# Optimization experiments

Measured on AMD Instinct MI355X. Metric: run time of the kernel, lower is better.

## Reference

```python
import jax, jax.numpy as jnp
import numpy as np
from jax import lax

B, T, I, H = 64, 512, 256, 512


def _lstm_cell(inp, h, c, Wx, bx, Wh):
    # Wx: (4, in_dim, H), bx: (4, H), Wh: (4, H, H); gate order: i, f, o, g
    gates = jnp.einsum('bi,gio->bgo', inp, Wx) + jnp.einsum('bh,gho->bgo', h, Wh) + bx
    i_t = jax.nn.sigmoid(gates[:, 0])
    f_t = jax.nn.sigmoid(gates[:, 1])
    o_t = jax.nn.sigmoid(gates[:, 2])
    g_t = jnp.tanh(gates[:, 3])
    c_new = f_t * c + i_t * g_t
    h_new = o_t * jnp.tanh(c_new)
    return h_new, c_new


def setup_inputs() -> dict:
    key = jax.random.key(0)
    ks = jax.random.split(key, 9)
    s_i = 1.0 / np.sqrt(H)  # nn.Linear default init scale (uniform fan_in)
    s_x0 = 1.0 / np.sqrt(I)
    u = lambda k, shape, s: jax.random.uniform(k, shape, jnp.float32, -s, s)
    return {
        'x':   jax.random.normal(ks[0], (B, T, I), jnp.float32),
        'Wx0': u(ks[1], (4, I, H), s_x0),
        'bx0': u(ks[2], (4, H), s_x0),
        'Wh0': u(ks[3], (4, H, H), s_i),
        'Wx1': u(ks[4], (4, H, H), s_i),
        'bx1': u(ks[5], (4, H), s_i),
        'Wh1': u(ks[6], (4, H, H), s_i),
        'Wfc': u(ks[7], (H, 1), s_i),
        'bfc': u(ks[8], (1,), s_i),
    }


def reference(x, Wx0, bx0, Wh0, Wx1, bx1, Wh1, Wfc, bfc):
    b = x.shape[0]
    h = Wh0.shape[-1]
    zeros = jnp.zeros((b, h), x.dtype)
    carry0 = (zeros, zeros, zeros, zeros)  # h0, c0, h1, c1

    def step(carry, x_t):
        h0, c0, h1, c1 = carry
        h0, c0 = _lstm_cell(x_t, h0, c0, Wx0, bx0, Wh0)
        h1, c1 = _lstm_cell(h0, h1, c1, Wx1, bx1, Wh1)
        return (h0, c0, h1, c1), None

    x_t_major = jnp.swapaxes(x, 0, 1)  # (T, B, I)
    (h0, c0, h1, c1), _ = lax.scan(step, carry0, x_t_major)
    return h1 @ Wfc + bfc  # (B, 1)
```

## Files before the change

kernel.cpp:

```cpp
#include <hip/hip_runtime.h>
#include <stdint.h>

#define B_ 64
#define T_ 512
#define I_ 256
#define H_ 512
#define NTHR_ 512
#define D_ 8

typedef __attribute__((ext_vector_type(8))) short short8;
typedef __attribute__((ext_vector_type(4))) float float4v;
typedef __attribute__((ext_vector_type(4))) unsigned int uint4v;

static_assert(sizeof(short8) == 16, "");

#define TILE_B 2048
#define SLOT_B ((size_t)4 * 16 * TILE_B)

__device__ __forceinline__ unsigned short f2bf(float x) {
  union { float f; uint32_t u; } v; v.f = x;
  uint32_t r = v.u + 0x7FFFu + ((v.u >> 16) & 1u);
  return (unsigned short)(r >> 16);
}
__device__ __forceinline__ float bf2f(unsigned short h) {
  union { uint32_t u; float f; } v; v.u = ((uint32_t)h) << 16; return v.f;
}
__device__ __forceinline__ void splitHL(float x, unsigned short& hi, unsigned short& lo) {
  hi = f2bf(x);
  lo = f2bf(x - bf2f(hi));
}

__device__ __forceinline__ size_t rbyte(int slot, int bg, int ht) {
  return ((size_t)slot * 64 + bg * 16 + ht) * TILE_B;
}

__device__ __forceinline__ void wait_ge(const uint32_t* p, int tgt) {
  if (tgt <= 0) return;
  int it = 0;
  while ((int)__hip_atomic_load(p, __ATOMIC_RELAXED, __HIP_MEMORY_SCOPE_AGENT) < tgt) {
    if (++it > 2000000) break;
    if (it > 32) __builtin_amdgcn_s_sleep(1);
  }
}

__device__ __forceinline__ short8 mk8(uint32_t a0, uint32_t a1, uint32_t b0, uint32_t b1) {
  union { uint32_t u[4]; short8 s; } t;
  t.u[0] = a0; t.u[1] = a1; t.u[2] = b0; t.u[3] = b1;
  return t.s;
}

#define MFMA16(A, Bv, C) __builtin_amdgcn_mfma_f32_16x16x32_bf16(A, Bv, C, 0, 0, 0)

#define WAITV(n) do { \
    asm volatile("s_waitcnt vmcnt(" #n ")" ::: "memory"); \
    __builtin_amdgcn_sched_barrier(0); \
  } while (0)

template <int LAYER, bool FULL, bool XPK>
__device__ void run_layer(
    int a,
    const float* __restrict__ x,
    const uint8_t* __restrict__ xpk,
    const float* __restrict__ Wxp, const float* __restrict__ bxp,
    const float* __restrict__ Whp,
    uint32_t* prog0, uint32_t* prog1,
    uint8_t* r0, uint8_t* r1,
    float* h1f,
    unsigned short* Wsh, float* red)
{
  constexpr int K1 = LAYER ? H_ : I_;
  constexpr int NT = (K1 + H_) / 32;
  constexpr int NTT = NT / 2;
  const int tid = threadIdx.x;
  const int lane = tid & 63;
  const int wid = tid >> 6;
  const int bg = wid & 3;
  const int kh = wid >> 2;
  const int qq = lane >> 4;
  const int cc = lane & 15;
  const int brow = bg * 16 + cc;

  short8 wlo[NTT];
  for (int pass = 0; pass < 2; ++pass) {
    for (int idx = tid; idx < NT * 512; idx += NTHR_) {
      int tile = idx >> 9, r = idx & 511, ln = r >> 3, j = r & 7;
      int k = tile * 32 + 4 * (ln >> 4) + (j & 3) + 16 * (j >> 2);
      int n = 4 * a + (ln & 3);
      int g = (ln & 15) >> 2;
      float wvv = (k < K1) ? Wxp[((size_t)g * K1 + k) * H_ + n]
                           : Whp[((size_t)g * H_ + (k - K1)) * H_ + n];
      unsigned short hi, lo; splitHL(wvv, hi, lo);
      Wsh[idx] = pass ? hi : lo;
    }
    __syncthreads();
    if (pass == 0) {
      #pragma unroll
      for (int tt = 0; tt < NTT; ++tt) {
        int tile = 2 * tt + kh;
        wlo[tt] = *(const short8*)(Wsh + tile * 512 + lane * 8);
      }
      __syncthreads();
    }
  }

  const float biasv = bxp[(size_t)(cc >> 2) * H_ + 4 * a + (cc & 3)];
  float cst[4] = {0.f, 0.f, 0.f, 0.f};

  uint32_t* myprog = LAYER ? prog1 : prog0;
  const bool ownw = FULL ? ((tid & 127) == a) : false;

  for (int t = 0; t < T_; ++t) {
    const int slotP = FULL ? t       : (t & (D_ - 1));
    const int slotC = FULL ? (t + 1) : ((t + 1) & (D_ - 1));
    const float bv = (kh == 0) ? biasv : 0.f;
    float4v accA = {bv, bv, bv, bv};
    float4v accB = {0.f, 0.f, 0.f, 0.f};
    float4v accC = {0.f, 0.f, 0.f, 0.f};

    uint4v X0[8], X1[8];

    auto issue_ring = [&](int tt) {
      const int tile = 2 * tt + kh;
      const uint8_t* p;
      if (!LAYER)         p = r0 + rbyte(slotP, bg, tile - 8);
      else if (tile < 16) p = r0 + rbyte(slotC, bg, tile);
      else                p = r1 + rbyte(slotP, bg, tile - 16);
      p += (size_t)lane * 16;
      const int s = tt & 7;
      if constexpr (FULL) {
        asm volatile("global_load_dwordx4 %0, %2, off\n\t"
                     "global_load_dwordx4 %1, %2, off offset:1024"
                     : "=&v"(X0[s]), "=&v"(X1[s]) : "v"(p) : "memory");
      } else {
        asm volatile("global_load_dwordx4 %0, %2, off sc0 sc1\n\t"
                     "global_load_dwordx4 %1, %2, off offset:1024 sc0 sc1"
                     : "=&v"(X0[s]), "=&v"(X1[s]) : "v"(p) : "memory");
      }
    };
    auto issue_x = [&](int tt) {
      const int tile = 2 * tt + kh;
      const uint8_t* p = xpk + (((size_t)t * 4 + bg) * 8 + tile) * TILE_B
                       + (size_t)lane * 16;
      const int s = tt & 7;
      asm volatile("global_load_dwordx4 %0, %2, off\n\t"
                   "global_load_dwordx4 %1, %2, off offset:1024"
                   : "=&v"(X0[s]), "=&v"(X1[s]) : "v"(p) : "memory");
    };
    auto proc_ring = [&](int tt) {
      const int tile = 2 * tt + kh;
      const int s = tt & 7;
      short8 h = mk8(X0[s][0], X0[s][1], X1[s][0], X1[s][1]);
      short8 l = mk8(X0[s][2], X0[s][3], X1[s][2], X1[s][3]);
      short8 bhi = *(const short8*)(Wsh + tile * 512 + lane * 8);
      accA = MFMA16(h, bhi, accA);
      accB = MFMA16(l, bhi, accB);
      accC = MFMA16(h, wlo[tt], accC);
    };

    if constexpr (!LAYER) {
      if constexpr (XPK) {
        #pragma unroll
        for (int tt = 0; tt < 4; ++tt) issue_x(tt);
        if constexpr (FULL) {
          if (!ownw) wait_ge(&prog0[tid], t);
        }
        __syncthreads();
        #pragma unroll
        for (int tt = 4; tt < 8; ++tt) issue_ring(tt);
        WAITV(8);
        proc_ring(0); proc_ring(1); proc_ring(2); proc_ring(3);
        issue_ring(8); issue_ring(9); issue_ring(10); issue_ring(11);
        WAITV(8);
        proc_ring(4); proc_ring(5); proc_ring(6); proc_ring(7);
        WAITV(0);
        proc_ring(8); proc_ring(9); proc_ring(10); proc_ring(11);
      } else {
        uint4v xw0[4], xw1[4];
        #pragma unroll
        for (int u = 0; u < 4; ++u) {
          const float* xp = x + ((size_t)brow * T_ + t) * I_ + (2 * u + kh) * 32 + 4 * qq;
          asm volatile("global_load_dwordx4 %0, %2, off\n\t"
                       "global_load_dwordx4 %1, %2, off offset:64"
                       : "=&v"(xw0[u]), "=&v"(xw1[u]) : "v"(xp) : "memory");
        }
        if constexpr (FULL) {
          if (!ownw) wait_ge(&prog0[tid], t);
        } else {
          if (tid < 128)      wait_ge(&prog0[tid], t);
          else if (tid < 256) wait_ge(&prog1[tid - 128], t - (D_ - 1));
        }
        __syncthreads();
        #pragma unroll
        for (int tt = 4; tt < 12; ++tt) issue_ring(tt);
        WAITV(16);
        #pragma unroll
        for (int u = 0; u < 4; ++u) {
          short8 ahi, alo;
          #pragma unroll
          for (int j = 0; j < 4; ++j) {
            unsigned short hh, ll;
            splitHL(__uint_as_float(xw0[u][j]), hh, ll); ahi[j] = (short)hh; alo[j] = (short)ll;
            splitHL(__uint_as_float(xw1[u][j]), hh, ll); ahi[j + 4] = (short)hh; alo[j + 4] = (short)ll;
          }
          const int tile = 2 * u + kh;
          short8 bhi = *(const short8*)(Wsh + tile * 512 + lane * 8);
          accA = MFMA16(ahi, bhi, accA);
          accB = MFMA16(alo, bhi, accB);
          accC = MFMA16(ahi, wlo[u], accC);
        }
        WAITV(8);
        proc_ring(4); proc_ring(5); proc_ring(6); proc_ring(7);
        WAITV(0);
        proc_ring(8); proc_ring(9); proc_ring(10); proc_ring(11);
      }
    } else {
      if constexpr (FULL) {
        wait_ge(&prog0[tid], t + 1);
        __syncthreads();
        #pragma unroll
        for (int tt = 0; tt < 8; ++tt) issue_ring(tt);
        if (!ownw) wait_ge(&prog1[tid], t);
        __syncthreads();
        WAITV(8);
        proc_ring(0); proc_ring(1); proc_ring(2); proc_ring(3);
        issue_ring(8); issue_ring(9); issue_ring(10); issue_ring(11);
        WAITV(8);
        proc_ring(4); proc_ring(5); proc_ring(6); proc_ring(7);
        issue_ring(12); issue_ring(13); issue_ring(14); issue_ring(15);
        WAITV(8);
        proc_ring(8); proc_ring(9); proc_ring(10); proc_ring(11);
        WAITV(0);
        proc_ring(12); proc_ring(13); proc_ring(14); proc_ring(15);
      } else {
        if (tid < 128)      wait_ge(&prog0[tid], t + 1);
        else if (tid < 256) wait_ge(&prog1[tid - 128], t);
        __syncthreads();
        #pragma unroll
        for (int tt = 0; tt < 8; ++tt) issue_ring(tt);
        WAITV(8);
        proc_ring(0); proc_ring(1); proc_ring(2); proc_ring(3);
        issue_ring(8); issue_ring(9); issue_ring(10); issue_ring(11);
        WAITV(8);
        proc_ring(4); proc_ring(5); proc_ring(6); proc_ring(7);
        issue_ring(12); issue_ring(13); issue_ring(14); issue_ring(15);
        WAITV(8);
        proc_ring(8); proc_ring(9); proc_ring(10); proc_ring(11);
        WAITV(0);
        proc_ring(12); proc_ring(13); proc_ring(14); proc_ring(15);
      }
    }

    float4v acc = accA + accB + accC;

    if (kh == 1) *(float4v*)(red + ((bg << 6) + lane) * 4) = acc;
    __syncthreads();
    if (kh == 0) {
      acc += *(const float4v*)(red + ((bg << 6) + lane) * 4);

      const bool isg = cc >= 12;
      float av[4];
      #pragma unroll
      for (int i = 0; i < 4; ++i) {
        float xg = acc[i];
        float arg = isg ? xg + xg : xg;
        float e = __expf(-fabsf(arg));
        float s = (arg >= 0.f) ? 1.f / (1.f + e) : e / (1.f + e);
        av[i] = isg ? (s + s - 1.f) : s;
      }
      float hn[4];
      #pragma unroll
      for (int i = 0; i < 4; ++i) {
        float fv = __shfl_xor(av[i], 4);
        float ov = __shfl_xor(av[i], 8);
        float gv = __shfl_xor(av[i], 12);
        float cn = fv * cst[i] + av[i] * gv;
        cst[i] = cn;
        float e2 = __expf(-2.f * fabsf(cn));
        float th = (1.f - e2) / (1.f + e2);
        hn[i] = ov * ((cn >= 0.f) ? th : -th);
      }
      float v0[4], v1[4], v2[4], v3[4];
      #pragma unroll
      for (int d = 0; d < 4; ++d) {
        int src = (lane & 0x30) | d;
        v0[d] = __shfl(hn[0], src);
        v1[d] = __shfl(hn[1], src);
        v2[d] = __shfl(hn[2], src);
        v3[d] = __shfl(hn[3], src);
      }
      if (cc < 4) {
        unsigned short hh[4], ll[4]; float4v hf;
        #pragma unroll
        for (int d = 0; d < 4; ++d) {
          float hv = (cc == 0) ? v0[d] : (cc == 1) ? v1[d] : (cc == 2) ? v2[d] : v3[d];
          hf[d] = hv;
          splitHL(hv, hh[d], ll[d]);
        }
        uint4v pk;
        pk[0] = (uint32_t)hh[0] | ((uint32_t)hh[1] << 16);
        pk[1] = (uint32_t)hh[2] | ((uint32_t)hh[3] << 16);
        pk[2] = (uint32_t)ll[0] | ((uint32_t)ll[1] << 16);
        pk[3] = (uint32_t)ll[2] | ((uint32_t)ll[3] << 16);
        uint8_t* dstb = (LAYER ? r1 : r0) + rbyte(slotC, bg, a >> 3)
                      + (size_t)((a >> 2) & 1) * 1024
                      + (size_t)(16 * (a & 3) + 4 * qq + cc) * 16;
        asm volatile("global_store_dwordx4 %0, %1, off sc0 sc1"
                     :: "v"(dstb), "v"(pk) : "memory");
        if (LAYER && t == T_ - 1) {
          float4v* hp = (float4v*)(h1f + (size_t)(bg * 16 + 4 * qq + cc) * H_ + 4 * a);
          asm volatile("global_store_dwordx4 %0, %1, off sc0 sc1"
                       :: "v"(hp), "v"(hf) : "memory");
        }
      }
    }
    if constexpr (FULL) {
      if (kh == 0) {
        asm volatile("s_waitcnt vmcnt(0)" ::: "memory");
        if (lane == 0)
          __hip_atomic_store(&myprog[bg * 128 + a], (uint32_t)(t + 1),
                             __ATOMIC_RELAXED, __HIP_MEMORY_SCOPE_AGENT);
      }
      __syncthreads();
    } else {
      asm volatile("s_waitcnt vmcnt(0)" ::: "memory");
      __syncthreads();
      if (tid == 0)
        __hip_atomic_store(&myprog[a], (uint32_t)(t + 1),
                           __ATOMIC_RELAXED, __HIP_MEMORY_SCOPE_AGENT);
    }
  }
}

template <bool FULL, bool XPK>
__global__ __launch_bounds__(NTHR_, 2) void lstm_persist(
    const float* __restrict__ x, const uint8_t* __restrict__ xpk,
    const float* __restrict__ Wx0, const float* __restrict__ bx0, const float* __restrict__ Wh0,
    const float* __restrict__ Wx1, const float* __restrict__ bx1, const float* __restrict__ Wh1,
    uint32_t* prog0, uint32_t* prog1,
    uint8_t* ring0, uint8_t* ring1,
    float* h1f)
{
  __shared__ unsigned short Wsh[16384];
  __shared__ float red[1024];
  if (blockIdx.x < 128)
    run_layer<0, FULL, XPK>(blockIdx.x, x, xpk, Wx0, bx0, Wh0, prog0, prog1,
                            ring0, ring1, h1f, Wsh, red);
  else
    run_layer<1, FULL, XPK>(blockIdx.x - 128, x, xpk, Wx1, bx1, Wh1, prog0, prog1,
                            ring0, ring1, h1f, Wsh, red);
}

__global__ void prep_x(const float* __restrict__ x, uint8_t* __restrict__ xpk)
{
  size_t idx = (size_t)blockIdx.x * blockDim.x + threadIdx.x;
  if (idx >= (size_t)T_ * 4 * 8 * 2 * 64) return;
  int l    = idx & 63;
  int jh   = (idx >> 6) & 1;
  int tile = (idx >> 7) & 7;
  int bg   = (idx >> 10) & 3;
  int t    = (int)(idx >> 12);
  int row  = bg * 16 + (l & 15);
  int k0   = tile * 32 + 4 * (l >> 4) + 16 * jh;
  float4v f = *(const float4v*)(x + ((size_t)row * T_ + t) * I_ + k0);
  unsigned short hh[4], ll[4];
  #pragma unroll
  for (int d = 0; d < 4; ++d) splitHL(f[d], hh[d], ll[d]);
  uint4v pk;
  pk[0] = (uint32_t)hh[0] | ((uint32_t)hh[1] << 16);
  pk[1] = (uint32_t)hh[2] | ((uint32_t)hh[3] << 16);
  pk[2] = (uint32_t)ll[0] | ((uint32_t)ll[1] << 16);
  pk[3] = (uint32_t)ll[2] | ((uint32_t)ll[3] << 16);
  *(uint4v*)(xpk + idx * 16) = pk;
}

__global__ void fc_out(const float* __restrict__ h1f, const float* __restrict__ Wfc,
                       const float* __restrict__ bfc, float* __restrict__ out)
{
  int tid = threadIdx.x;
  int b = tid >> 3, p = tid & 7;
  const float* hp = h1f + (size_t)b * H_ + p * 64;
  const float* wp = Wfc + p * 64;
  float4v hv[16];
  #pragma unroll
  for (int q = 0; q < 16; ++q)
    asm volatile("global_load_dwordx4 %0, %1, off sc0 sc1"
                 : "=&v"(hv[q]) : "v"(hp + 4 * q) : "memory");
  asm volatile("s_waitcnt vmcnt(0)" ::: "memory");
  float s = 0.f;
  #pragma unroll
  for (int q = 0; q < 16; ++q) {
    float4v wv = *(const float4v*)(wp + 4 * q);
    s += hv[q][0] * wv[0] + hv[q][1] * wv[1] + hv[q][2] * wv[2] + hv[q][3] * wv[3];
  }
  s += __shfl_xor(s, 1);
  s += __shfl_xor(s, 2);
  s += __shfl_xor(s, 4);
  if (p == 0) out[b] = s + bfc[0];
}

extern "C" void kernel_launch(void* const* d_in, const int* in_sizes, int n_in,
                              void* d_out, int out_size, void* d_ws, size_t ws_size,
                              hipStream_t stream)
{
  const float* x   = (const float*)d_in[0];
  const float* Wx0 = (const float*)d_in[1];
  const float* bx0 = (const float*)d_in[2];
  const float* Wh0 = (const float*)d_in[3];
  const float* Wx1 = (const float*)d_in[4];
  const float* bx1 = (const float*)d_in[5];
  const float* Wh1 = (const float*)d_in[6];
  const float* Wfc = (const float*)d_in[7];
  const float* bfc = (const float*)d_in[8];

  uint8_t* ws = (uint8_t*)d_ws;
  const size_t RINGB_FULL = (size_t)(T_ + 1) * SLOT_B;
  const size_t RINGB_CYC  = (size_t)D_ * SLOT_B;
  const size_t XPKB       = (size_t)T_ * 4 * 8 * TILE_B;
  const size_t H1FB       = (size_t)B_ * H_ * 4;
  const size_t NEED_FULL  = 4096 + 2 * RINGB_FULL + H1FB;
  const size_t NEED_XPK   = NEED_FULL + XPKB;

  uint32_t* prog0 = (uint32_t*)ws;
  uint32_t* prog1 = (uint32_t*)(ws + 2048);

  if (ws_size >= NEED_XPK) {
    uint8_t* ring0 = ws + 4096;
    uint8_t* ring1 = ws + 4096 + RINGB_FULL;
    uint8_t* xpk   = ws + 4096 + 2 * RINGB_FULL;
    float* h1f = (float*)(ws + 4096 + 2 * RINGB_FULL + XPKB);
    (void)hipMemsetAsync(ws, 0, 4096 + SLOT_B, stream);
    (void)hipMemsetAsync(ring1, 0, SLOT_B, stream);
    hipLaunchKernelGGL(prep_x, dim3(4096), dim3(512), 0, stream, x, xpk);
    hipLaunchKernelGGL((lstm_persist<true, true>), dim3(256), dim3(NTHR_), 0, stream,
                       x, xpk, Wx0, bx0, Wh0, Wx1, bx1, Wh1,
                       prog0, prog1, ring0, ring1, h1f);
    hipLaunchKernelGGL(fc_out, dim3(1), dim3(512), 0, stream,
                       h1f, Wfc, bfc, (float*)d_out);
  } else if (ws_size >= NEED_FULL) {
    uint8_t* ring0 = ws + 4096;
    uint8_t* ring1 = ws + 4096 + RINGB_FULL;
    float* h1f = (float*)(ws + 4096 + 2 * RINGB_FULL);
    (void)hipMemsetAsync(ws, 0, 4096 + SLOT_B, stream);
    (void)hipMemsetAsync(ring1, 0, SLOT_B, stream);
    hipLaunchKernelGGL((lstm_persist<true, false>), dim3(256), dim3(NTHR_), 0, stream,
                       x, (const uint8_t*)nullptr, Wx0, bx0, Wh0, Wx1, bx1, Wh1,
                       prog0, prog1, ring0, ring1, h1f);
    hipLaunchKernelGGL(fc_out, dim3(1), dim3(512), 0, stream,
                       h1f, Wfc, bfc, (float*)d_out);
  } else {
    uint8_t* ring0 = ws + 4096;
    uint8_t* ring1 = ws + 4096 + RINGB_CYC;
    float* h1f = (float*)(ws + 4096 + 2 * RINGB_CYC);
    (void)hipMemsetAsync(ws, 0, 4096 + 2 * RINGB_CYC, stream);
    hipLaunchKernelGGL((lstm_persist<false, false>), dim3(256), dim3(NTHR_), 0, stream,
                       x, (const uint8_t*)nullptr, Wx0, bx0, Wh0, Wx1, bx1, Wh1,
                       prog0, prog1, ring0, ring1, h1f);
    hipLaunchKernelGGL(fc_out, dim3(1), dim3(512), 0, stream,
                       h1f, Wfc, bfc, (float*)d_out);
  }
}
```

Before: 2.749 ms.

## Replace block-wide flag waits with per-wave group polling and double-buffer reduction

In the FULL path each wave now polls only the progress flags of its own batch group: every lane does one 64-bit load covering two flags and the wave leaves when all lanes see them ready. This replaces the per-thread waits followed by __syncthreads. The trailing __syncthreads after publishing progress is removed, and the partial-sum reduction buffer in shared memory is double-buffered by step parity so the next step's write cannot race the current read. The goal is fewer block-wide barriers on the recurrent critical path between dependent blocks. The cost is that waves can drift apart, so correctness now rests on the parity buffering and on per-group flag dependencies.

```diff
diff --git a/kernel.cpp b/kernel.cpp
--- a/kernel.cpp
+++ b/kernel.cpp
@@ -39,6 +39,21 @@
   int it = 0;
   while ((int)__hip_atomic_load(p, __ATOMIC_RELAXED, __HIP_MEMORY_SCOPE_AGENT) < tgt) {
     if (++it > 2000000) break;
+    if (it > 32) __builtin_amdgcn_s_sleep(1);
+  }
+}
+
+__device__ __forceinline__ void pollg(const uint32_t* grp, int tgt) {
+  if (tgt <= 0) return;
+  const int lane = threadIdx.x & 63;
+  const unsigned long long* p = (const unsigned long long*)grp + lane;
+  int it = 0;
+  while (true) {
+    unsigned long long v = __hip_atomic_load(p, __ATOMIC_RELAXED,
+                                             __HIP_MEMORY_SCOPE_AGENT);
+    bool ok = ((int)(uint32_t)v >= tgt) && ((int)(uint32_t)(v >> 32) >= tgt);
+    if (__all((int)ok)) return;
+    if (++it > 2000000) return;
     if (it > 32) __builtin_amdgcn_s_sleep(1);
   }
 }
@@ -107,7 +122,8 @@
   float cst[4] = {0.f, 0.f, 0.f, 0.f};
 
   uint32_t* myprog = LAYER ? prog1 : prog0;
-  const bool ownw = FULL ? ((tid & 127) == a) : false;
+  const uint32_t* g0 = prog0 + bg * 128;
+  const uint32_t* g1 = prog1 + bg * 128;
 
   for (int t = 0; t < T_; ++t) {
     const int slotP = FULL ? t       : (t & (D_ - 1));
@@ -158,13 +174,10 @@
     };
 
     if constexpr (!LAYER) {
-      if constexpr (XPK) {
+      if constexpr (XPK && FULL) {
         #pragma unroll
         for (int tt = 0; tt < 4; ++tt) issue_x(tt);
-        if constexpr (FULL) {
-          if (!ownw) wait_ge(&prog0[tid], t);
-        }
-        __syncthreads();
+        pollg(g0, t);
         #pragma unroll
         for (int tt = 4; tt < 8; ++tt) issue_ring(tt);
         WAITV(8);
@@ -174,7 +187,7 @@
         proc_ring(4); proc_ring(5); proc_ring(6); proc_ring(7);
         WAITV(0);
         proc_ring(8); proc_ring(9); proc_ring(10); proc_ring(11);
-      } else {
+      } else if constexpr (FULL) {
         uint4v xw0[4], xw1[4];
         #pragma unroll
         for (int u = 0; u < 4; ++u) {
@@ -183,13 +196,7 @@
                        "global_load_dwordx4 %1, %2, off offset:64"
                        : "=&v"(xw0[u]), "=&v"(xw1[u]) : "v"(xp) : "memory");
         }
-        if constexpr (FULL) {
-          if (!ownw) wait_ge(&prog0[tid], t);
-        } else {
-          if (tid < 128)      wait_ge(&prog0[tid], t);
-          else if (tid < 256) wait_ge(&prog1[tid - 128], t - (D_ - 1));
-        }
-        __syncthreads();
+        pollg(g0, t);
         #pragma unroll
         for (int tt = 4; tt < 12; ++tt) issue_ring(tt);
         WAITV(16);
@@ -212,15 +219,47 @@
         proc_ring(4); proc_ring(5); proc_ring(6); proc_ring(7);
         WAITV(0);
         proc_ring(8); proc_ring(9); proc_ring(10); proc_ring(11);
+      } else {
+        uint4v xw0[4], xw1[4];
+        #pragma unroll
+        for (int u = 0; u < 4; ++u) {
+          const float* xp = x + ((size_t)brow * T_ + t) * I_ + (2 * u + kh) * 32 + 4 * qq;
+          asm volatile("global_load_dwordx4 %0, %2, off\n\t"
+                       "global_load_dwordx4 %1, %2, off offset:64"
+                       : "=&v"(xw0[u]), "=&v"(xw1[u]) : "v"(xp) : "memory");
+        }
+        if (tid < 128)      wait_ge(&prog0[tid], t);
+        else if (tid < 256) wait_ge(&prog1[tid - 128], t - (D_ - 1));
+        __syncthreads();
+        #pragma unroll
+        for (int tt = 4; tt < 12; ++tt) issue_ring(tt);
+        WAITV(16);
+        #pragma unroll
+        for (int u = 0; u < 4; ++u) {
+          short8 ahi, alo;
+          #pragma unroll
+          for (int j = 0; j < 4; ++j) {
+            unsigned short hh, ll;
+            splitHL(__uint_as_float(xw0[u][j]), hh, ll); ahi[j] = (short)hh; alo[j] = (short)ll;
+            splitHL(__uint_as_float(xw1[u][j]), hh, ll); ahi[j + 4] = (short)hh; alo[j + 4] = (short)ll;
+          }
+          const int tile = 2 * u + kh;
+          short8 bhi = *(const short8*)(Wsh + tile * 512 + lane * 8);
+          accA = MFMA16(ahi, bhi, accA);
+          accB = MFMA16(alo, bhi, accB);
+          accC = MFMA16(ahi, wlo[u], accC);
+        }
+        WAITV(8);
+        proc_ring(4); proc_ring(5); proc_ring(6); proc_ring(7);
+        WAITV(0);
+        proc_ring(8); proc_ring(9); proc_ring(10); proc_ring(11);
       }
     } else {
       if constexpr (FULL) {
-        wait_ge(&prog0[tid], t + 1);
-        __syncthreads();
+        pollg(g0, t + 1);
         #pragma unroll
         for (int tt = 0; tt < 8; ++tt) issue_ring(tt);
-        if (!ownw) wait_ge(&prog1[tid], t);
-        __syncthreads();
+        pollg(g1, t);
         WAITV(8);
         proc_ring(0); proc_ring(1); proc_ring(2); proc_ring(3);
         issue_ring(8); issue_ring(9); issue_ring(10); issue_ring(11);
@@ -252,10 +291,11 @@
 
     float4v acc = accA + accB + accC;
 
-    if (kh == 1) *(float4v*)(red + ((bg << 6) + lane) * 4) = acc;
+    float* redp = red + ((t & 1) << 10);
+    if (kh == 1) *(float4v*)(redp + ((bg << 6) + lane) * 4) = acc;
     __syncthreads();
     if (kh == 0) {
-      acc += *(const float4v*)(red + ((bg << 6) + lane) * 4);
+      acc += *(const float4v*)(redp + ((bg << 6) + lane) * 4);
 
       const bool isg = cc >= 12;
       float av[4];
@@ -312,16 +352,14 @@
                        :: "v"(hp), "v"(hf) : "memory");
         }
       }
-    }
-    if constexpr (FULL) {
-      if (kh == 0) {
+      if constexpr (FULL) {
         asm volatile("s_waitcnt vmcnt(0)" ::: "memory");
         if (lane == 0)
           __hip_atomic_store(&myprog[bg * 128 + a], (uint32_t)(t + 1),
                              __ATOMIC_RELAXED, __HIP_MEMORY_SCOPE_AGENT);
       }
-      __syncthreads();
-    } else {
+    }
+    if constexpr (!FULL) {
       asm volatile("s_waitcnt vmcnt(0)" ::: "memory");
       __syncthreads();
       if (tid == 0)
@@ -341,7 +379,7 @@
     float* h1f)
 {
   __shared__ unsigned short Wsh[16384];
-  __shared__ float red[1024];
+  __shared__ float red[2048];
   if (blockIdx.x < 128)
     run_layer<0, FULL, XPK>(blockIdx.x, x, xpk, Wx0, bx0, Wh0, prog0, prog1,
                             ring0, ring1, h1f, Wsh, red);
```

Result: slower. 4.198 ms (+52.7%).
